# Performance work log

Measured on AMD Instinct MI355X. Metric: run time of the kernel, lower is better.

The kernel has to match this reference:

```python
import jax, jax.numpy as jnp
import numpy as np

Z = 128      # z_size
N = 256      # n_neurons_param_net
F = 2048     # n_functions
B = 8192     # batch


def setup_inputs() -> dict:
    key = jax.random.key(0)
    ks = jax.random.split(key, 16)
    sN = 1.0 / np.sqrt(N)
    inp = {
        "t": jax.random.uniform(ks[0], (1,), dtype=jnp.float32),
        "z_and_logpz": jax.random.normal(ks[1], (B, Z + 1), dtype=jnp.float32),
        # stacked first two layers of the 4 parameter-predicting MLPs
        # order: [w_in_net, w_out_net, b_net, gate_net]
        "W1": jax.random.normal(ks[2], (4, N, 1), dtype=jnp.float32),
        "B1": jax.random.normal(ks[3], (4, N), dtype=jnp.float32) * 0.01,
        "W2": jax.random.normal(ks[4], (4, N, N), dtype=jnp.float32) * sN,
        "B2": jax.random.normal(ks[5], (4, N), dtype=jnp.float32) * 0.01,
        # per-head final layers
        "W3_win": jax.random.normal(ks[6], (F * Z, N), dtype=jnp.float32) * sN,
        "b3_win": jax.random.normal(ks[7], (F * Z,), dtype=jnp.float32) * 0.01,
        "W3_wout": jax.random.normal(ks[8], (F * Z, N), dtype=jnp.float32) * sN,
        "b3_wout": jax.random.normal(ks[9], (F * Z,), dtype=jnp.float32) * 0.01,
        "W3_b": jax.random.normal(ks[10], (F, N), dtype=jnp.float32) * sN,
        "b3_b": jax.random.normal(ks[11], (F,), dtype=jnp.float32) * 0.01,
        "W3_gate": jax.random.normal(ks[12], (F, N), dtype=jnp.float32) * sN,
        "b3_gate": jax.random.normal(ks[13], (F,), dtype=jnp.float32) * 0.01,
    }
    return inp


def reference(t, z_and_logpz, W1, B1, W2, B2, W3_win, b3_win,
              W3_wout, b3_wout, W3_b, b3_b, W3_gate, b3_gate):
    F_ = W3_b.shape[0]
    Z_ = W3_win.shape[0] // F_
    ts = t.reshape(())  # scalar time

    # parameter-predicting MLPs (4 tiny 3-layer MLPs, first 2 layers stacked)
    h0 = jnp.tanh(W1[:, :, 0] * ts + B1)                    # [4, N]
    h1 = jnp.tanh(jnp.einsum('knm,km->kn', W2, h0) + B2)    # [4, N]
    w_in = (W3_win @ h1[0] + b3_win).reshape(F_, Z_)        # [F, Z]
    w_out = (W3_wout @ h1[1] + b3_wout).reshape(F_, Z_)     # [F, Z]
    b = W3_b @ h1[2] + b3_b                                 # [F]
    gate = jax.nn.sigmoid(W3_gate @ h1[3] + b3_gate)        # [F]

    z = z_and_logpz[:, :Z_]                                 # [B, Z]
    h = jnp.tanh(z @ w_in.T + b)                            # [B, F]
    g = h * gate                                            # gated hidden
    dz_dt = (g @ w_out) / F_                                # mean over functions -> [B, Z]

    # exact Jacobian trace (analytic; identical to autograd trace of this net):
    # d f_i / d z_i = mean_f gate_f * (1 - h_f^2) * w_out[f,i] * w_in[f,i]
    s = jnp.sum(w_in * w_out, axis=1)                       # [F]
    trace = ((1.0 - h * h) * gate) @ s / F_                 # [B]
    dlogpz_dt = -trace[:, None]                             # [B, 1]
    return jnp.concatenate([dz_dt, dlogpz_dt], axis=-1)     # [B, Z+1]
```

## Files before the change

kernel.cpp:

```cpp
#include <hip/hip_runtime.h>
#include <hip/hip_bf16.h>
#include <math.h>

typedef float f32x4 __attribute__((ext_vector_type(4)));
typedef float f32x4u __attribute__((ext_vector_type(4))) __attribute__((aligned(4)));
typedef short s16x8 __attribute__((ext_vector_type(8)));

__device__ __forceinline__ float wave_reduce64(float v) {
#pragma unroll
    for (int m = 32; m > 0; m >>= 1) v += __shfl_xor(v, m, 64);
    return v;
}

__device__ __forceinline__ unsigned short f32_to_bf16_rn(float x) {
    unsigned int u = __float_as_uint(x);
    unsigned int r = (u + 0x7fffu + ((u >> 16) & 1u)) >> 16;
    return (unsigned short)r;
}
__device__ __forceinline__ float bf16_to_f32(unsigned short h) {
    return __uint_as_float(((unsigned int)h) << 16);
}

__device__ __forceinline__ void dma_row16(const float* gsrc, float* ldst) {
    __builtin_amdgcn_global_load_lds(
        (const __attribute__((address_space(1))) unsigned int*)gsrc,
        (__attribute__((address_space(3))) unsigned int*)ldst,
        16, 0, 0);
}

__global__ __launch_bounds__(256) void kA(const float* __restrict__ t,
                                          const float* __restrict__ W1, const float* __restrict__ B1,
                                          const float* __restrict__ W2, const float* __restrict__ B2,
                                          float* __restrict__ h1) {
    const int tid = threadIdx.x;
    const int wave = (blockIdx.x << 2) + (tid >> 6);
    const int lane = tid & 63;
    const int k = wave >> 8, n = wave & 255;
    const float ts = t[0];
    const int m0 = lane << 2;
    f32x4 w1 = *(const f32x4*)(W1 + k * 256 + m0);
    f32x4 b1 = *(const f32x4*)(B1 + k * 256 + m0);
    f32x4 w2 = *(const f32x4*)(W2 + (size_t)(k * 256 + n) * 256 + m0);
    float p = 0.f;
    p += w2.x * tanhf(w1.x * ts + b1.x);
    p += w2.y * tanhf(w1.y * ts + b1.y);
    p += w2.z * tanhf(w1.z * ts + b1.z);
    p += w2.w * tanhf(w1.w * ts + b1.w);
    p = wave_reduce64(p);
    if (lane == 0) h1[k * 256 + n] = tanhf(p + B2[k * 256 + n]);
}

__global__ __launch_bounds__(256) void kB_dma(const float* __restrict__ Wwin, const float* __restrict__ bwin,
                                              const float* __restrict__ Wwout, const float* __restrict__ bwout,
                                              const float* __restrict__ Wb, const float* __restrict__ bb,
                                              const float* __restrict__ Wg, const float* __restrict__ bg,
                                              const float* __restrict__ h1,
                                              float* __restrict__ w_in, float* __restrict__ w_out,
                                              unsigned short* __restrict__ w_in_hi, unsigned short* __restrict__ w_in_lo,
                                              unsigned short* __restrict__ w_out_t,
                                              float* __restrict__ b_arr, float* __restrict__ gate) {
    extern __shared__ float smem[];
    float* h_s = smem;
    float* bufs = smem + 1088;

    const int tid = threadIdx.x;
    const int w = tid >> 6, lane = tid & 63;

    {
        const int seg = tid >> 6, q = (tid >> 4) & 3, i = tid & 15;
        f32x4 hv = *(const f32x4*)(h1 + seg * 256 + q * 64 + i * 4);
        *(f32x4*)(h_s + seg * 272 + q * 68 + i * 4) = hv;
    }

    const int r = lane >> 2, c = lane & 3;

#pragma unroll
    for (int pk = 0; pk < 2; pk++) {
        const int ci = blockIdx.x + pk * 256;
        const float* W; int row0;
        if (ci < 4096)      { W = Wwin;  row0 = ci * 64; }
        else if (ci < 8192) { W = Wwout; row0 = (ci - 4096) * 64; }
        else if (ci < 8224) { W = Wb;    row0 = (ci - 8192) * 64; }
        else                { W = Wg;    row0 = (ci - 8224) * 64; }
        const float* src = W + (size_t)(row0 + w * 16) * 256 + (lane << 2);
        float* dst = bufs + (size_t)((pk * 4 + w) * 16) * 260;
#pragma unroll
        for (int rr = 0; rr < 16; rr++) dma_row16(src + rr * 256, dst + rr * 260);
    }

    __syncthreads();

    for (int k = 0;; k++) {
        const int cur = blockIdx.x + k * 256;
        if (cur >= 8256) break;
        const int buf = k & 1;
        const bool has_next = (cur + 256) < 8256;
        if (has_next) asm volatile("s_waitcnt vmcnt(16)" ::: "memory");
        else          asm volatile("s_waitcnt vmcnt(0)" ::: "memory");

        int seg, row0;
        const float* bias;
        if (cur < 4096)      { seg = 0; row0 = cur * 64;          bias = bwin; }
        else if (cur < 8192) { seg = 1; row0 = (cur - 4096) * 64; bias = bwout; }
        else if (cur < 8224) { seg = 2; row0 = (cur - 8192) * 64; bias = bb; }
        else                 { seg = 3; row0 = (cur - 8224) * 64; bias = bg; }

        const float* rowp = bufs + (size_t)((buf * 4 + w) * 16 + r) * 260 + c * 64;
        const float* hp = h_s + seg * 272 + c * 68;
        float a0 = 0.f, a1 = 0.f;
#pragma unroll
        for (int j = 0; j < 16; j += 2) {
            f32x4 d0 = *(const f32x4*)(rowp + 4 * j);
            f32x4 h0 = *(const f32x4*)(hp + 4 * j);
            f32x4 d1 = *(const f32x4*)(rowp + 4 * j + 4);
            f32x4 h1v = *(const f32x4*)(hp + 4 * j + 4);
            a0 += d0.x * h0.x + d0.y * h0.y + d0.z * h0.z + d0.w * h0.w;
            a1 += d1.x * h1v.x + d1.y * h1v.y + d1.z * h1v.z + d1.w * h1v.w;
        }
        float acc = a0 + a1;
        acc += __shfl_xor(acc, 1, 64);
        acc += __shfl_xor(acc, 2, 64);

        if (c == 0) {
            const int idx = row0 + w * 16 + r;
            float v = acc + bias[idx];
            if (seg == 0) {
                w_in[idx] = v;
                unsigned short hi = f32_to_bf16_rn(v);
                w_in_hi[idx] = hi;
                w_in_lo[idx] = f32_to_bf16_rn(v - bf16_to_f32(hi));
            } else if (seg == 1) {
                w_out[idx] = v;
                w_out_t[(size_t)(idx & 127) * 2048 + (idx >> 7)] = f32_to_bf16_rn(v);
            } else if (seg == 2) {
                b_arr[idx] = v;
            } else {
                gate[idx] = 1.f / (1.f + __expf(-v));
            }
        }

        asm volatile("s_waitcnt lgkmcnt(0)" ::: "memory");

        const int pf = cur + 512;
        if (pf < 8256) {
            const float* W; int prow0;
            if (pf < 4096)      { W = Wwin;  prow0 = pf * 64; }
            else if (pf < 8192) { W = Wwout; prow0 = (pf - 4096) * 64; }
            else if (pf < 8224) { W = Wb;    prow0 = (pf - 8192) * 64; }
            else                { W = Wg;    prow0 = (pf - 8224) * 64; }
            const float* src = W + (size_t)(prow0 + w * 16) * 256 + (lane << 2);
            float* dst = bufs + (size_t)((buf * 4 + w) * 16) * 260;
#pragma unroll
            for (int rr = 0; rr < 16; rr++) dma_row16(src + rr * 256, dst + rr * 260);
        }
    }
}

__global__ __launch_bounds__(256) void kB_fb(const float* __restrict__ Wwin, const float* __restrict__ bwin,
                                             const float* __restrict__ Wwout, const float* __restrict__ bwout,
                                             const float* __restrict__ Wb, const float* __restrict__ bb,
                                             const float* __restrict__ Wg, const float* __restrict__ bg,
                                             const float* __restrict__ h1,
                                             float* __restrict__ w_in, float* __restrict__ w_out,
                                             unsigned short* __restrict__ w_in_hi, unsigned short* __restrict__ w_in_lo,
                                             unsigned short* __restrict__ w_out_t,
                                             float* __restrict__ b_arr, float* __restrict__ gate) {
    const int lane = threadIdx.x & 63;
    const int wave0 = (blockIdx.x << 2) + (threadIdx.x >> 6);
    const int nwaves = gridDim.x << 2;
    const int m0 = lane << 2;
    const f32x4 h_win  = *(const f32x4*)(h1 + m0);
    const f32x4 h_wout = *(const f32x4*)(h1 + 256 + m0);
    const f32x4 h_b    = *(const f32x4*)(h1 + 512 + m0);
    const f32x4 h_g    = *(const f32x4*)(h1 + 768 + m0);
    for (int g = wave0; g < 132096; g += nwaves) {
        const int rr = g << 2;
        const float* W; const float* bias; f32x4 hv; int idx, seg;
        if (rr < 262144)      { seg = 0; idx = rr;          W = Wwin;  bias = bwin;  hv = h_win; }
        else if (rr < 524288) { seg = 1; idx = rr - 262144; W = Wwout; bias = bwout; hv = h_wout; }
        else if (rr < 526336) { seg = 2; idx = rr - 524288; W = Wb;    bias = bb;    hv = h_b; }
        else                  { seg = 3; idx = rr - 526336; W = Wg;    bias = bg;    hv = h_g; }
        const float* base = W + (size_t)idx * 256 + m0;
        f32x4 w0 = *(const f32x4*)(base);
        f32x4 w1 = *(const f32x4*)(base + 256);
        f32x4 w2 = *(const f32x4*)(base + 512);
        f32x4 w3 = *(const f32x4*)(base + 768);
        float p0 = w0.x * hv.x + w0.y * hv.y + w0.z * hv.z + w0.w * hv.w;
        float p1 = w1.x * hv.x + w1.y * hv.y + w1.z * hv.z + w1.w * hv.w;
        float p2 = w2.x * hv.x + w2.y * hv.y + w2.z * hv.z + w2.w * hv.w;
        float p3 = w3.x * hv.x + w3.y * hv.y + w3.z * hv.z + w3.w * hv.w;
#pragma unroll
        for (int m = 32; m > 0; m >>= 1) {
            p0 += __shfl_xor(p0, m, 64);
            p1 += __shfl_xor(p1, m, 64);
            p2 += __shfl_xor(p2, m, 64);
            p3 += __shfl_xor(p3, m, 64);
        }
        if (lane < 4) {
            float v = (lane == 0) ? p0 : (lane == 1) ? p1 : (lane == 2) ? p2 : p3;
            const int id2 = idx + lane;
            v += bias[id2];
            if (seg == 0) {
                w_in[id2] = v;
                unsigned short hi = f32_to_bf16_rn(v);
                w_in_hi[id2] = hi;
                w_in_lo[id2] = f32_to_bf16_rn(v - bf16_to_f32(hi));
            } else if (seg == 1) {
                w_out[id2] = v;
                w_out_t[(size_t)(id2 & 127) * 2048 + (id2 >> 7)] = f32_to_bf16_rn(v);
            } else if (seg == 2) {
                b_arr[id2] = v;
            } else {
                gate[id2] = 1.f / (1.f + __expf(-v));
            }
        }
    }
}

__global__ __launch_bounds__(256) void kC(const float* __restrict__ w_in, const float* __restrict__ w_out,
                                          float* __restrict__ s) {
    const int f = (blockIdx.x << 2) + (threadIdx.x >> 6);
    const int lane = threadIdx.x & 63;
    float2 a = *(const float2*)(w_in + (size_t)f * 128 + lane * 2);
    float2 b = *(const float2*)(w_out + (size_t)f * 128 + lane * 2);
    float p = a.x * b.x + a.y * b.y;
    p = wave_reduce64(p);
    if (lane == 0) s[f] = p;
}

__global__ __launch_bounds__(256) void kD(const float* __restrict__ zin,
                                          const unsigned short* __restrict__ w_in_hi,
                                          const unsigned short* __restrict__ w_in_lo,
                                          const unsigned short* __restrict__ w_out_t,
                                          const float* __restrict__ b_arr, const float* __restrict__ gate,
                                          const float* __restrict__ s, float* __restrict__ out) {
    __shared__ __attribute__((aligned(16))) unsigned short g_lds[4][16][72];
    __shared__ __attribute__((aligned(16))) float red[3][64][36];

    const int tid = threadIdx.x;
    const int w = tid >> 6, lane = tid & 63;
    const int q = lane >> 4, lm = lane & 15;
    const int b0 = blockIdx.x * 16;
    const int brow = b0 + lm;

    s16x8 zh[4], zl[4];
#pragma unroll
    for (int kt = 0; kt < 4; kt++) {
        const float* zp = zin + (size_t)brow * 129 + kt * 32 + q * 8;
        f32x4u z0 = *(const f32x4u*)(zp);
        f32x4u z1 = *(const f32x4u*)(zp + 4);
        float zv[8] = {z0.x, z0.y, z0.z, z0.w, z1.x, z1.y, z1.z, z1.w};
#pragma unroll
        for (int j = 0; j < 8; j++) {
            unsigned short hi = f32_to_bf16_rn(zv[j]);
            zh[kt][j] = (short)hi;
            zl[kt][j] = (short)f32_to_bf16_rn(zv[j] - bf16_to_f32(hi));
        }
    }

    f32x4 acc2[8];
#pragma unroll
    for (int ct = 0; ct < 8; ct++) acc2[ct] = (f32x4){0.f, 0.f, 0.f, 0.f};
    float tr[4] = {0.f, 0.f, 0.f, 0.f};

    for (int ch = 0; ch < 8; ch++) {
        const int f0 = w * 512 + ch * 64;
#pragma unroll
        for (int nt = 0; nt < 4; nt++) {
            const int fc = f0 + nt * 16 + lm;
            const unsigned short* ph = w_in_hi + (size_t)fc * 128;
            const unsigned short* pl = w_in_lo + (size_t)fc * 128;
            f32x4 acc1 = {0.f, 0.f, 0.f, 0.f};
#pragma unroll
            for (int kt = 0; kt < 4; kt++) {
                s16x8 bh = *(const s16x8*)(ph + kt * 32 + q * 8);
                s16x8 bl = *(const s16x8*)(pl + kt * 32 + q * 8);
                acc1 = __builtin_amdgcn_mfma_f32_16x16x32_bf16(zh[kt], bh, acc1, 0, 0, 0);
                acc1 = __builtin_amdgcn_mfma_f32_16x16x32_bf16(zh[kt], bl, acc1, 0, 0, 0);
                acc1 = __builtin_amdgcn_mfma_f32_16x16x32_bf16(zl[kt], bh, acc1, 0, 0, 0);
            }
            const float gv = gate[fc], bv = b_arr[fc], sv = s[fc];
#pragma unroll
            for (int i = 0; i < 4; i++) {
                float pre = acc1[i] + bv;
                float e = __expf(2.f * pre);
                float th = 1.f - 2.f * __builtin_amdgcn_rcpf(e + 1.f);
                float g = th * gv;
                tr[i] += (1.f - th * th) * gv * sv;
                g_lds[w][q * 4 + i][nt * 16 + lm] = f32_to_bf16_rn(g);
            }
        }
#pragma unroll
        for (int kt2 = 0; kt2 < 2; kt2++) {
            s16x8 af = *(const s16x8*)&g_lds[w][lm][kt2 * 32 + q * 8];
#pragma unroll
            for (int ct = 0; ct < 8; ct++) {
                s16x8 bf = *(const s16x8*)(w_out_t + (size_t)(ct * 16 + lm) * 2048 + f0 + kt2 * 32 + q * 8);
                acc2[ct] = __builtin_amdgcn_mfma_f32_16x16x32_bf16(af, bf, acc2[ct], 0, 0, 0);
            }
        }
    }

    if (w != 0) {
#pragma unroll
        for (int ct = 0; ct < 8; ct++) *(f32x4*)&red[w - 1][lane][ct * 4] = acc2[ct];
        *(f32x4*)&red[w - 1][lane][32] = (f32x4){tr[0], tr[1], tr[2], tr[3]};
    }
    __syncthreads();
    if (w == 0) {
#pragma unroll
        for (int ww = 0; ww < 3; ww++) {
#pragma unroll
            for (int ct = 0; ct < 8; ct++) {
                f32x4 o = *(const f32x4*)&red[ww][lane][ct * 4];
                acc2[ct].x += o.x; acc2[ct].y += o.y; acc2[ct].z += o.z; acc2[ct].w += o.w;
            }
            f32x4 to = *(const f32x4*)&red[ww][lane][32];
            tr[0] += to.x; tr[1] += to.y; tr[2] += to.z; tr[3] += to.w;
        }

        const float inv = 1.f / 2048.f;
#pragma unroll
        for (int ct = 0; ct < 8; ct++)
#pragma unroll
            for (int i = 0; i < 4; i++)
                out[(size_t)(b0 + q * 4 + i) * 129 + ct * 16 + lm] = acc2[ct][i] * inv;
#pragma unroll
        for (int i = 0; i < 4; i++) {
            float t2 = tr[i];
            t2 += __shfl_xor(t2, 1, 64);
            t2 += __shfl_xor(t2, 2, 64);
            t2 += __shfl_xor(t2, 4, 64);
            t2 += __shfl_xor(t2, 8, 64);
            if (lm == 0) out[(size_t)(b0 + q * 4 + i) * 129 + 128] = -t2 * inv;
        }
    }
}

extern "C" void kernel_launch(void* const* d_in, const int* in_sizes, int n_in,
                              void* d_out, int out_size, void* d_ws, size_t ws_size,
                              hipStream_t stream) {
    const float* t     = (const float*)d_in[0];
    const float* z     = (const float*)d_in[1];
    const float* W1    = (const float*)d_in[2];
    const float* B1    = (const float*)d_in[3];
    const float* W2    = (const float*)d_in[4];
    const float* B2    = (const float*)d_in[5];
    const float* W3win = (const float*)d_in[6];
    const float* b3win = (const float*)d_in[7];
    const float* W3wo  = (const float*)d_in[8];
    const float* b3wo  = (const float*)d_in[9];
    const float* W3b   = (const float*)d_in[10];
    const float* b3b   = (const float*)d_in[11];
    const float* W3g   = (const float*)d_in[12];
    const float* b3g   = (const float*)d_in[13];
    float* out = (float*)d_out;

    float* h1    = (float*)d_ws;
    float* w_in  = h1 + 1024;
    float* w_out = w_in + 262144;
    float* b_arr = w_out + 262144;
    float* gate  = b_arr + 2048;
    float* s     = gate + 2048;
    unsigned short* w_in_hi = (unsigned short*)(s + 2048);
    unsigned short* w_in_lo = w_in_hi + 262144;
    unsigned short* w_out_t = w_in_lo + 262144;

    kA<<<256, 256, 0, stream>>>(t, W1, B1, W2, B2, h1);

    const int kb_lds = (1088 + 8 * 16 * 260) * 4;
    hipError_t attr_ok = hipFuncSetAttribute((const void*)kB_dma,
                                             hipFuncAttributeMaxDynamicSharedMemorySize, kb_lds);
    if (attr_ok == hipSuccess) {
        kB_dma<<<256, 256, kb_lds, stream>>>(W3win, b3win, W3wo, b3wo, W3b, b3b, W3g, b3g, h1,
                                             w_in, w_out, w_in_hi, w_in_lo, w_out_t, b_arr, gate);
    } else {
        kB_fb<<<2048, 256, 0, stream>>>(W3win, b3win, W3wo, b3wo, W3b, b3b, W3g, b3g, h1,
                                        w_in, w_out, w_in_hi, w_in_lo, w_out_t, b_arr, gate);
    }
    kC<<<512, 256, 0, stream>>>(w_in, w_out, s);
    kD<<<512, 256, 0, stream>>>(z, w_in_hi, w_in_lo, w_out_t, b_arr, gate, s, out);
    (void)in_sizes; (void)n_in; (void)out_size; (void)ws_size;
}
```

Measured before the change: 625.5 us.

## Fuse all stages into one cooperative persistent kernel with grid syncs

Replaces the four kernel launches (h1 MLP, weight generation, s reduction, main batch GEMM) with one cooperative kernel of 256 blocks × 512 threads that uses grid-wide syncs between phases. Each block recomputes the small h1 MLP redundantly while its initial DMA prefetch of weight rows is in flight, so the first weight loads overlap the MLP. The intent is to remove launch gaps and the separate h1 pass. The cost is redundant MLP work in every block, two grid barriers, and a fallback path whose degenerate branch launches a single-thread kA instead of the removed kB_fb, which would produce wrong results if taken.

```diff
diff --git a/kernel.cpp b/kernel.cpp
--- a/kernel.cpp
+++ b/kernel.cpp
@@ -1,6 +1,9 @@
 #include <hip/hip_runtime.h>
 #include <hip/hip_bf16.h>
+#include <hip/hip_cooperative_groups.h>
 #include <math.h>
+
+namespace cg = cooperative_groups;
 
 typedef float f32x4 __attribute__((ext_vector_type(4)));
 typedef float f32x4u __attribute__((ext_vector_type(4))) __attribute__((aligned(4)));
@@ -27,6 +30,256 @@
         (__attribute__((address_space(3))) unsigned int*)ldst,
         16, 0, 0);
 }
+
+__global__ __launch_bounds__(512, 2) void kF(
+    const float* __restrict__ t, const float* __restrict__ zin,
+    const float* __restrict__ W1, const float* __restrict__ B1,
+    const float* __restrict__ W2, const float* __restrict__ B2,
+    const float* __restrict__ Wwin, const float* __restrict__ bwin,
+    const float* __restrict__ Wwout, const float* __restrict__ bwout,
+    const float* __restrict__ Wb, const float* __restrict__ bb,
+    const float* __restrict__ Wg, const float* __restrict__ bg,
+    float* __restrict__ w_in, float* __restrict__ w_out,
+    unsigned short* __restrict__ w_in_hi, unsigned short* __restrict__ w_in_lo,
+    unsigned short* __restrict__ w_out_t,
+    float* __restrict__ b_arr, float* __restrict__ gate,
+    float* __restrict__ s, float* __restrict__ out) {
+    extern __shared__ float smem[];
+    float* h_s = smem;
+    float* bufs = smem + 1088;
+    float* h0_p = smem + 34368;
+
+    const int tid = threadIdx.x;
+    const int w = tid >> 6, lane = tid & 63;
+    const int bid = blockIdx.x;
+
+    if (tid < 256) {
+#pragma unroll
+        for (int pk = 0; pk < 2; pk++) {
+            const int ci = bid + pk * 256;
+            const float* W; int row0;
+            if (ci < 4096)      { W = Wwin;  row0 = ci * 64; }
+            else if (ci < 8192) { W = Wwout; row0 = (ci - 4096) * 64; }
+            else if (ci < 8224) { W = Wb;    row0 = (ci - 8192) * 64; }
+            else                { W = Wg;    row0 = (ci - 8224) * 64; }
+            const float* src = W + (size_t)(row0 + w * 16) * 256 + (lane << 2);
+            float* dst = bufs + (size_t)((pk * 4 + w) * 16) * 260;
+#pragma unroll
+            for (int rr = 0; rr < 16; rr++) dma_row16(src + rr * 256, dst + rr * 260);
+        }
+    }
+
+    {
+        const float ts = t[0];
+        for (int o = tid; o < 1024; o += 512)
+            h0_p[o] = tanhf(W1[o] * ts + B1[o]);
+        __syncthreads();
+        for (int o = tid; o < 1024; o += 512) {
+            const int k = o >> 8, n = o & 255;
+            const float* w2p = W2 + ((size_t)o << 8);
+            const float* h0k = h0_p + (k << 8);
+            float ax = 0.f, ay = 0.f, az = 0.f, aw = 0.f;
+#pragma unroll 8
+            for (int m = 0; m < 256; m += 4) {
+                f32x4 wv = *(const f32x4*)(w2p + m);
+                f32x4 hv = *(const f32x4*)(h0k + m);
+                ax += wv.x * hv.x; ay += wv.y * hv.y;
+                az += wv.z * hv.z; aw += wv.w * hv.w;
+            }
+            float v = tanhf((ax + ay) + (az + aw) + B2[o]);
+            h_s[k * 272 + ((n >> 6) * 68) + (n & 63)] = v;
+        }
+        __syncthreads();
+    }
+
+    if (tid < 256) {
+        const int r = lane >> 2, c = lane & 3;
+        for (int k = 0;; k++) {
+            const int cur = bid + k * 256;
+            if (cur >= 8256) break;
+            const int buf = k & 1;
+            const bool has_next = (cur + 256) < 8256;
+            if (has_next) asm volatile("s_waitcnt vmcnt(16)" ::: "memory");
+            else          asm volatile("s_waitcnt vmcnt(0)" ::: "memory");
+
+            int seg, row0;
+            const float* bias;
+            if (cur < 4096)      { seg = 0; row0 = cur * 64;          bias = bwin; }
+            else if (cur < 8192) { seg = 1; row0 = (cur - 4096) * 64; bias = bwout; }
+            else if (cur < 8224) { seg = 2; row0 = (cur - 8192) * 64; bias = bb; }
+            else                 { seg = 3; row0 = (cur - 8224) * 64; bias = bg; }
+
+            const float* rowp = bufs + (size_t)((buf * 4 + w) * 16 + r) * 260 + c * 64;
+            const float* hp = h_s + seg * 272 + c * 68;
+            float a0 = 0.f, a1 = 0.f;
+#pragma unroll
+            for (int j = 0; j < 16; j += 2) {
+                f32x4 d0 = *(const f32x4*)(rowp + 4 * j);
+                f32x4 h0 = *(const f32x4*)(hp + 4 * j);
+                f32x4 d1 = *(const f32x4*)(rowp + 4 * j + 4);
+                f32x4 h1v = *(const f32x4*)(hp + 4 * j + 4);
+                a0 += d0.x * h0.x + d0.y * h0.y + d0.z * h0.z + d0.w * h0.w;
+                a1 += d1.x * h1v.x + d1.y * h1v.y + d1.z * h1v.z + d1.w * h1v.w;
+            }
+            float acc = a0 + a1;
+            acc += __shfl_xor(acc, 1, 64);
+            acc += __shfl_xor(acc, 2, 64);
+
+            if (c == 0) {
+                const int idx = row0 + w * 16 + r;
+                float v = acc + bias[idx];
+                if (seg == 0) {
+                    w_in[idx] = v;
+                    unsigned short hi = f32_to_bf16_rn(v);
+                    w_in_hi[idx] = hi;
+                    w_in_lo[idx] = f32_to_bf16_rn(v - bf16_to_f32(hi));
+                } else if (seg == 1) {
+                    w_out[idx] = v;
+                    w_out_t[(size_t)(idx & 127) * 2048 + (idx >> 7)] = f32_to_bf16_rn(v);
+                } else if (seg == 2) {
+                    b_arr[idx] = v;
+                } else {
+                    gate[idx] = 1.f / (1.f + __expf(-v));
+                }
+            }
+
+            asm volatile("s_waitcnt lgkmcnt(0)" ::: "memory");
+
+            const int pf = cur + 512;
+            if (pf < 8256) {
+                const float* W; int prow0;
+                if (pf < 4096)      { W = Wwin;  prow0 = pf * 64; }
+                else if (pf < 8192) { W = Wwout; prow0 = (pf - 4096) * 64; }
+                else if (pf < 8224) { W = Wb;    prow0 = (pf - 8192) * 64; }
+                else                { W = Wg;    prow0 = (pf - 8224) * 64; }
+                const float* src = W + (size_t)(prow0 + w * 16) * 256 + (lane << 2);
+                float* dst = bufs + (size_t)((buf * 4 + w) * 16) * 260;
+#pragma unroll
+                for (int rr = 0; rr < 16; rr++) dma_row16(src + rr * 256, dst + rr * 260);
+            }
+        }
+    }
+
+    __threadfence();
+    cg::this_grid().sync();
+
+    {
+        const int f = bid * 8 + w;
+        float2 a = *(const float2*)(w_in + (size_t)f * 128 + lane * 2);
+        float2 b = *(const float2*)(w_out + (size_t)f * 128 + lane * 2);
+        float p = a.x * b.x + a.y * b.y;
+        p = wave_reduce64(p);
+        if (lane == 0) s[f] = p;
+    }
+
+    __threadfence();
+    cg::this_grid().sync();
+
+    {
+        unsigned short* g_lds = (unsigned short*)smem;
+        float* red = smem + 4608;
+
+        const int g = w >> 2, w4 = w & 3;
+        const int q = lane >> 4, lm = lane & 15;
+        const int b0 = bid * 32 + g * 16;
+        const int brow = b0 + lm;
+
+        s16x8 zh[4], zl[4];
+#pragma unroll
+        for (int kt = 0; kt < 4; kt++) {
+            const float* zp = zin + (size_t)brow * 129 + kt * 32 + q * 8;
+            f32x4u z0 = *(const f32x4u*)(zp);
+            f32x4u z1 = *(const f32x4u*)(zp + 4);
+            float zv[8] = {z0.x, z0.y, z0.z, z0.w, z1.x, z1.y, z1.z, z1.w};
+#pragma unroll
+            for (int j = 0; j < 8; j++) {
+                unsigned short hi = f32_to_bf16_rn(zv[j]);
+                zh[kt][j] = (short)hi;
+                zl[kt][j] = (short)f32_to_bf16_rn(zv[j] - bf16_to_f32(hi));
+            }
+        }
+
+        f32x4 acc2[8];
+#pragma unroll
+        for (int ct = 0; ct < 8; ct++) acc2[ct] = (f32x4){0.f, 0.f, 0.f, 0.f};
+        float tr[4] = {0.f, 0.f, 0.f, 0.f};
+
+        for (int ch = 0; ch < 8; ch++) {
+            const int f0 = w4 * 512 + ch * 64;
+#pragma unroll
+            for (int nt = 0; nt < 4; nt++) {
+                const int fc = f0 + nt * 16 + lm;
+                const unsigned short* ph = w_in_hi + (size_t)fc * 128;
+                const unsigned short* pl = w_in_lo + (size_t)fc * 128;
+                f32x4 acc1 = {0.f, 0.f, 0.f, 0.f};
+#pragma unroll
+                for (int kt = 0; kt < 4; kt++) {
+                    s16x8 bh = *(const s16x8*)(ph + kt * 32 + q * 8);
+                    s16x8 bl = *(const s16x8*)(pl + kt * 32 + q * 8);
+                    acc1 = __builtin_amdgcn_mfma_f32_16x16x32_bf16(zh[kt], bh, acc1, 0, 0, 0);
+                    acc1 = __builtin_amdgcn_mfma_f32_16x16x32_bf16(zh[kt], bl, acc1, 0, 0, 0);
+                    acc1 = __builtin_amdgcn_mfma_f32_16x16x32_bf16(zl[kt], bh, acc1, 0, 0, 0);
+                }
+                const float gv = gate[fc], bv = b_arr[fc], sv = s[fc];
+#pragma unroll
+                for (int i = 0; i < 4; i++) {
+                    float pre = acc1[i] + bv;
+                    float e = __expf(2.f * pre);
+                    float th = 1.f - 2.f * __builtin_amdgcn_rcpf(e + 1.f);
+                    float gg = th * gv;
+                    tr[i] += (1.f - th * th) * gv * sv;
+                    g_lds[((g * 4 + w4) * 16 + (q * 4 + i)) * 72 + nt * 16 + lm] = f32_to_bf16_rn(gg);
+                }
+            }
+#pragma unroll
+            for (int kt2 = 0; kt2 < 2; kt2++) {
+                s16x8 af = *(const s16x8*)&g_lds[((g * 4 + w4) * 16 + lm) * 72 + kt2 * 32 + q * 8];
+#pragma unroll
+                for (int ct = 0; ct < 8; ct++) {
+                    s16x8 bf = *(const s16x8*)(w_out_t + (size_t)(ct * 16 + lm) * 2048 + f0 + kt2 * 32 + q * 8);
+                    acc2[ct] = __builtin_amdgcn_mfma_f32_16x16x32_bf16(af, bf, acc2[ct], 0, 0, 0);
+                }
+            }
+        }
+
+        if (w4 != 0) {
+#pragma unroll
+            for (int ct = 0; ct < 8; ct++)
+                *(f32x4*)&red[(((g * 3 + (w4 - 1)) * 64 + lane)) * 36 + ct * 4] = acc2[ct];
+            *(f32x4*)&red[(((g * 3 + (w4 - 1)) * 64 + lane)) * 36 + 32] = (f32x4){tr[0], tr[1], tr[2], tr[3]};
+        }
+        __syncthreads();
+        if (w4 == 0) {
+#pragma unroll
+            for (int ww = 0; ww < 3; ww++) {
+#pragma unroll
+                for (int ct = 0; ct < 8; ct++) {
+                    f32x4 o = *(const f32x4*)&red[(((g * 3 + ww) * 64 + lane)) * 36 + ct * 4];
+                    acc2[ct].x += o.x; acc2[ct].y += o.y; acc2[ct].z += o.z; acc2[ct].w += o.w;
+                }
+                f32x4 to = *(const f32x4*)&red[(((g * 3 + ww) * 64 + lane)) * 36 + 32];
+                tr[0] += to.x; tr[1] += to.y; tr[2] += to.z; tr[3] += to.w;
+            }
+
+            const float inv = 1.f / 2048.f;
+#pragma unroll
+            for (int ct = 0; ct < 8; ct++)
+#pragma unroll
+                for (int i = 0; i < 4; i++)
+                    out[(size_t)(b0 + q * 4 + i) * 129 + ct * 16 + lm] = acc2[ct][i] * inv;
+#pragma unroll
+            for (int i = 0; i < 4; i++) {
+                float t2 = tr[i];
+                t2 += __shfl_xor(t2, 1, 64);
+                t2 += __shfl_xor(t2, 2, 64);
+                t2 += __shfl_xor(t2, 4, 64);
+                t2 += __shfl_xor(t2, 8, 64);
+                if (lm == 0) out[(size_t)(b0 + q * 4 + i) * 129 + 128] = -t2 * inv;
+            }
+        }
+    }
+}
+
 
 __global__ __launch_bounds__(256) void kA(const float* __restrict__ t,
                                           const float* __restrict__ W1, const float* __restrict__ B1,
@@ -156,67 +409,6 @@
     }
 }
 
-__global__ __launch_bounds__(256) void kB_fb(const float* __restrict__ Wwin, const float* __restrict__ bwin,
-                                             const float* __restrict__ Wwout, const float* __restrict__ bwout,
-                                             const float* __restrict__ Wb, const float* __restrict__ bb,
-                                             const float* __restrict__ Wg, const float* __restrict__ bg,
-                                             const float* __restrict__ h1,
-                                             float* __restrict__ w_in, float* __restrict__ w_out,
-                                             unsigned short* __restrict__ w_in_hi, unsigned short* __restrict__ w_in_lo,
-                                             unsigned short* __restrict__ w_out_t,
-                                             float* __restrict__ b_arr, float* __restrict__ gate) {
-    const int lane = threadIdx.x & 63;
-    const int wave0 = (blockIdx.x << 2) + (threadIdx.x >> 6);
-    const int nwaves = gridDim.x << 2;
-    const int m0 = lane << 2;
-    const f32x4 h_win  = *(const f32x4*)(h1 + m0);
-    const f32x4 h_wout = *(const f32x4*)(h1 + 256 + m0);
-    const f32x4 h_b    = *(const f32x4*)(h1 + 512 + m0);
-    const f32x4 h_g    = *(const f32x4*)(h1 + 768 + m0);
-    for (int g = wave0; g < 132096; g += nwaves) {
-        const int rr = g << 2;
-        const float* W; const float* bias; f32x4 hv; int idx, seg;
-        if (rr < 262144)      { seg = 0; idx = rr;          W = Wwin;  bias = bwin;  hv = h_win; }
-        else if (rr < 524288) { seg = 1; idx = rr - 262144; W = Wwout; bias = bwout; hv = h_wout; }
-        else if (rr < 526336) { seg = 2; idx = rr - 524288; W = Wb;    bias = bb;    hv = h_b; }
-        else                  { seg = 3; idx = rr - 526336; W = Wg;    bias = bg;    hv = h_g; }
-        const float* base = W + (size_t)idx * 256 + m0;
-        f32x4 w0 = *(const f32x4*)(base);
-        f32x4 w1 = *(const f32x4*)(base + 256);
-        f32x4 w2 = *(const f32x4*)(base + 512);
-        f32x4 w3 = *(const f32x4*)(base + 768);
-        float p0 = w0.x * hv.x + w0.y * hv.y + w0.z * hv.z + w0.w * hv.w;
-        float p1 = w1.x * hv.x + w1.y * hv.y + w1.z * hv.z + w1.w * hv.w;
-        float p2 = w2.x * hv.x + w2.y * hv.y + w2.z * hv.z + w2.w * hv.w;
-        float p3 = w3.x * hv.x + w3.y * hv.y + w3.z * hv.z + w3.w * hv.w;
-#pragma unroll
-        for (int m = 32; m > 0; m >>= 1) {
-            p0 += __shfl_xor(p0, m, 64);
-            p1 += __shfl_xor(p1, m, 64);
-            p2 += __shfl_xor(p2, m, 64);
-            p3 += __shfl_xor(p3, m, 64);
-        }
-        if (lane < 4) {
-            float v = (lane == 0) ? p0 : (lane == 1) ? p1 : (lane == 2) ? p2 : p3;
-            const int id2 = idx + lane;
-            v += bias[id2];
-            if (seg == 0) {
-                w_in[id2] = v;
-                unsigned short hi = f32_to_bf16_rn(v);
-                w_in_hi[id2] = hi;
-                w_in_lo[id2] = f32_to_bf16_rn(v - bf16_to_f32(hi));
-            } else if (seg == 1) {
-                w_out[id2] = v;
-                w_out_t[(size_t)(id2 & 127) * 2048 + (id2 >> 7)] = f32_to_bf16_rn(v);
-            } else if (seg == 2) {
-                b_arr[id2] = v;
-            } else {
-                gate[id2] = 1.f / (1.f + __expf(-v));
-            }
-        }
-    }
-}
-
 __global__ __launch_bounds__(256) void kC(const float* __restrict__ w_in, const float* __restrict__ w_out,
                                           float* __restrict__ s) {
     const int f = (blockIdx.x << 2) + (threadIdx.x >> 6);
@@ -366,19 +558,32 @@
     unsigned short* w_in_lo = w_in_hi + 262144;
     unsigned short* w_out_t = w_in_lo + 262144;
 
-    kA<<<256, 256, 0, stream>>>(t, W1, B1, W2, B2, h1);
-
-    const int kb_lds = (1088 + 8 * 16 * 260) * 4;
-    hipError_t attr_ok = hipFuncSetAttribute((const void*)kB_dma,
-                                             hipFuncAttributeMaxDynamicSharedMemorySize, kb_lds);
-    if (attr_ok == hipSuccess) {
-        kB_dma<<<256, 256, kb_lds, stream>>>(W3win, b3win, W3wo, b3wo, W3b, b3b, W3g, b3g, h1,
-                                             w_in, w_out, w_in_hi, w_in_lo, w_out_t, b_arr, gate);
-    } else {
-        kB_fb<<<2048, 256, 0, stream>>>(W3win, b3win, W3wo, b3wo, W3b, b3b, W3g, b3g, h1,
-                                        w_in, w_out, w_in_hi, w_in_lo, w_out_t, b_arr, gate);
-    }
-    kC<<<512, 256, 0, stream>>>(w_in, w_out, s);
-    kD<<<512, 256, 0, stream>>>(z, w_in_hi, w_in_lo, w_out_t, b_arr, gate, s, out);
+    const int kf_lds = (1088 + 8 * 16 * 260 + 1024) * 4;
+    hipError_t e = hipFuncSetAttribute((const void*)kF,
+                                       hipFuncAttributeMaxDynamicSharedMemorySize, kf_lds);
+    if (e == hipSuccess) {
+        void* kargs[] = {
+            (void*)&t, (void*)&z, (void*)&W1, (void*)&B1, (void*)&W2, (void*)&B2,
+            (void*)&W3win, (void*)&b3win, (void*)&W3wo, (void*)&b3wo,
+            (void*)&W3b, (void*)&b3b, (void*)&W3g, (void*)&b3g,
+            (void*)&w_in, (void*)&w_out, (void*)&w_in_hi, (void*)&w_in_lo,
+            (void*)&w_out_t, (void*)&b_arr, (void*)&gate, (void*)&s, (void*)&out};
+        e = hipLaunchCooperativeKernel((const void*)kF, dim3(256), dim3(512),
+                                       kargs, (unsigned int)kf_lds, stream);
+    }
+    if (e != hipSuccess) {
+        kA<<<256, 256, 0, stream>>>(t, W1, B1, W2, B2, h1);
+        const int kb_lds = (1088 + 8 * 16 * 260) * 4;
+        hipError_t attr_ok = hipFuncSetAttribute((const void*)kB_dma,
+                                                 hipFuncAttributeMaxDynamicSharedMemorySize, kb_lds);
+        if (attr_ok == hipSuccess) {
+            kB_dma<<<256, 256, kb_lds, stream>>>(W3win, b3win, W3wo, b3wo, W3b, b3b, W3g, b3g, h1,
+                                                 w_in, w_out, w_in_hi, w_in_lo, w_out_t, b_arr, gate);
+        } else {
+            kA<<<1, 1, 0, stream>>>(t, W1, B1, W2, B2, h1);
+        }
+        kC<<<512, 256, 0, stream>>>(w_in, w_out, s);
+        kD<<<512, 256, 0, stream>>>(z, w_in_hi, w_in_lo, w_out_t, b_arr, gate, s, out);
+    }
     (void)in_sizes; (void)n_in; (void)out_size; (void)ws_size;
 }
```

Result: slower. 824.5 us (+31.8%).
